# Optimization experiments

Hardware: AMD Instinct MI355X
Metric: run time of the kernel (lower is better)

Reference implementation:

```python
import jax, jax.numpy as jnp
import numpy as np

B, H, CI, O = 8, 16, 16, 16          # batch, child spatial, child caps, parent caps
K, S, ROUTINGS = 3, 1, 3             # kernel, stride, EM iterations
FINAL_LAMBDA = 0.01
EPS = 1e-9


def setup_inputs() -> dict:
    key = jax.random.key(0)
    k1, k2, k3, k4, k5 = jax.random.split(key, 5)
    inputs_pose = jax.random.normal(k1, (B, H, H, CI, 16), dtype=jnp.float32)
    inputs_activation = jax.random.uniform(k2, (B, H, H, CI, 1), dtype=jnp.float32)
    # transformation matrices: [1, k*k*child_caps, parent_caps, 4, 4]
    w = jax.random.normal(k3, (1, K * K * CI, O, 4, 4), dtype=jnp.float32)
    beta_a = jax.random.normal(k4, (O,), dtype=jnp.float32)
    beta_v = jax.random.normal(k5, (O,), dtype=jnp.float32)
    return {"inputs_pose": inputs_pose, "inputs_activation": inputs_activation,
            "w": w, "beta_a": beta_a, "beta_v": beta_v}


def _extract_patches(x, k, s):
    # kernel_tile: im2col-like gather. x: [B, H, W, ...] -> [B, p, p, k, k, ...]
    Hs = x.shape[1]
    p = (Hs - k) // s + 1
    idx = (jnp.arange(p) * s)[:, None] + jnp.arange(k)[None, :]      # [p, k]
    xh = x[:, idx]                   # [B, ph, kh, W, ...]
    patches = xh[:, :, :, idx]       # [B, ph, kh, pw, kw, ...]
    return jnp.swapaxes(patches, 2, 3), p


def _child_index_map(Hs, k, s, p):
    # flat child spatial index feeding each (parent pos, kernel slot)
    ph = np.arange(p)[:, None] * s + np.arange(k)[None, :]           # [p, k]
    ch = ph[:, None, :, None] * Hs + ph[None, :, None, :]            # [p, p, k, k]
    return ch.reshape(p * p, k * k)                                   # [P2, K2]


def reference(inputs_pose, inputs_activation, w, beta_a, beta_v):
    P = (H - K) // S + 1
    P2, K2 = P * P, K * K
    K2CI = K2 * CI

    # ---- kernel_tile ----
    pose_t, _ = _extract_patches(inputs_pose, K, S)       # [B,P,P,K,K,CI,16]
    act_t, _ = _extract_patches(inputs_activation, K, S)  # [B,P,P,K,K,CI,1]
    pose_unroll = pose_t.reshape(B * P2, K2CI, 4, 4)
    act_unroll = act_t.reshape(B * P2, K2CI)

    # ---- compute_votes: tiny 4x4 matmuls per (child slot, parent cap) ----
    votes = jnp.einsum('nkpq,koqr->nkopr', pose_unroll, w[0])  # [B*P2,K2CI,O,4,4]
    votes = votes.reshape(B, P2, K2CI, O, 16)
    act_i = act_unroll.reshape(B, P2, K2CI, 1, 1)

    # ---- spatial routing bookkeeping (static integers) ----
    child_idx = _child_index_map(H, K, S, P)                    # [P2, K2]
    kk_child = np.repeat(child_idx, CI, axis=1)                 # [P2, K2CI]
    counts = np.zeros(H * H, np.float32)
    np.add.at(counts, child_idx.reshape(-1), 1.0)               # parents per child pos
    cap_id = np.tile(np.arange(CI), K2)                         # [K2CI]
    seg = jnp.asarray((kk_child * CI + cap_id[None, :]).reshape(-1))  # [P2*K2CI]
    n_seg = H * H * CI

    # initial routing: uniform over all (parent pos, parent cap) each child feeds
    rr0 = 1.0 / (O * counts[kk_child])                          # [P2, K2CI]
    rr = jnp.asarray(rr0)[None, :, :, None, None]               # bcast [1,P2,K2CI,1,1]

    beta_a_b = beta_a.reshape(1, 1, 1, O, 1)
    beta_v_b = beta_v.reshape(1, 1, 1, O, 1)

    mean = act_j = None
    for it in range(ROUTINGS):
        inv_temp = FINAL_LAMBDA * (1.0 - 0.95 ** (it + 1))
        # ---- M-step: weighted Gaussian statistics ----
        rr_prime = rr * act_i                                   # [B,P2,K2CI,O,1]
        rr_sum = jnp.sum(rr_prime, axis=2, keepdims=True) + EPS # [B,P2,1,O,1]
        mean = jnp.sum(rr_prime * votes, axis=2, keepdims=True) / rr_sum
        var = jnp.sum(rr_prime * jnp.square(votes - mean), axis=2, keepdims=True) / rr_sum + EPS
        cost_h = (beta_v_b + 0.5 * jnp.log(var)) * rr_sum       # [B,P2,1,O,16]
        cost = jnp.sum(cost_h, axis=-1, keepdims=True)          # [B,P2,1,O,1]
        act_j = jax.nn.sigmoid(inv_temp * (beta_a_b - cost))    # [B,P2,1,O,1]
        # ---- E-step: softmax over all (parent pos, parent cap) per child capsule ----
        if it < ROUTINGS - 1:
            log_p = -0.5 * jnp.sum(jnp.square(votes - mean) / var
                                   + jnp.log(2.0 * np.pi * var), axis=-1)  # [B,P2,K2CI,O]
            zz = jnp.log(act_j[..., 0] + EPS) + log_p           # [B,P2,K2CI,O]
            z = jnp.transpose(zz, (1, 2, 0, 3)).reshape(P2 * K2CI, B, O)
            row_max = jnp.max(z, axis=-1)                       # [P2*K2CI, B]
            seg_max = jax.ops.segment_max(row_max, seg, num_segments=n_seg)
            g = seg_max[seg][..., None]
            ez = jnp.exp(z - g)
            denom = jax.ops.segment_sum(jnp.sum(ez, axis=-1), seg, num_segments=n_seg)[seg]
            rr_new = ez / (denom[..., None] + EPS)              # sums to 1 per child capsule
            rr = jnp.transpose(rr_new.reshape(P2, K2CI, B, O), (2, 0, 1, 3))[..., None]

    pose_out = mean[:, :, 0].reshape(B, P, P, O, 16)
    act_out = act_j[:, :, 0].reshape(B, P, P, O, 1)
    return pose_out, act_out
```

## Files before the change

### kernel.cpp

```cpp
#include <hip/hip_runtime.h>

namespace {
constexpr int B_ = 8, H_ = 16, CI_ = 16, O_ = 16, P_ = 14;
constexpr int P2_ = P_ * P_;
constexpr int K2CI_ = 144;
constexpr int NV_ = 2304;
constexpr float EPS_ = 1e-9f;
constexpr float LOG2PI_ = 1.8378770664093453f;

using f2 = __attribute__((ext_vector_type(2))) float;

__device__ __forceinline__ float cnt1(int h) {
  int lo = (h - (P_ - 1)) > 0 ? (h - (P_ - 1)) : 0;
  int hi = h < 2 ? h : 2;
  return (float)(hi - lo + 1);
}

__global__ __launch_bounds__(256) void transpose_w(const float* __restrict__ w,
                                                   float* __restrict__ wt) {
  const int i = blockIdx.x * 256 + threadIdx.x;
  const int ko = i >> 4, q = (i >> 2) & 3, r = i & 3;
  wt[(ko << 4) + (r << 2) + q] = w[i];
}

__global__ __launch_bounds__(256) void transpose_pose(const float* __restrict__ pose,
                                                      float* __restrict__ pose_t) {
  const int i = blockIdx.x * 256 + threadIdx.x;
  const int cell = i >> 4, idx = i & 15;
  const int p = idx >> 2, q = idx & 3;
  pose_t[(cell << 4) + (q << 2) + p] = pose[i];
}

__device__ __forceinline__ void vote_dot(const float* __restrict__ pb, const float4 w4,
                                         f2& v01, f2& v23) {
  const f2 A0 = *(const f2*)(pb + 0), B0 = *(const f2*)(pb + 2);
  const f2 A1 = *(const f2*)(pb + 4), B1 = *(const f2*)(pb + 6);
  const f2 A2 = *(const f2*)(pb + 8), B2 = *(const f2*)(pb + 10);
  const f2 A3 = *(const f2*)(pb + 12), B3 = *(const f2*)(pb + 14);
  v01 = A0 * w4.x;
  v23 = B0 * w4.x;
  v01 = __builtin_elementwise_fma(A1, (f2){w4.y, w4.y}, v01);
  v23 = __builtin_elementwise_fma(B1, (f2){w4.y, w4.y}, v23);
  v01 = __builtin_elementwise_fma(A2, (f2){w4.z, w4.z}, v01);
  v23 = __builtin_elementwise_fma(B2, (f2){w4.z, w4.z}, v23);
  v01 = __builtin_elementwise_fma(A3, (f2){w4.w, w4.w}, v01);
  v23 = __builtin_elementwise_fma(B3, (f2){w4.w, w4.w}, v23);
}

template <int MODE>
__global__ __launch_bounds__(512, 8) void caps_main(
    const float* __restrict__ pose_t, const float* __restrict__ act,
    const float* __restrict__ wt, const float* __restrict__ beta_a,
    const float* __restrict__ beta_v, const float* __restrict__ zin,
    const float* __restrict__ gmax, const float* __restrict__ gden,
    float* __restrict__ zout, float* __restrict__ out) {
  __shared__ float rr_s[(MODE == 0) ? K2CI_ : NV_];
  __shared__ f2 partv[4][512];
  __shared__ float partr[512];
  __shared__ f2 sfin[4][64];
  __shared__ float sfr[64];
  __shared__ float gm_s[(MODE == 0) ? 1 : K2CI_];
  __shared__ float ad_s[(MODE == 0) ? 1 : K2CI_];

  const int tid = threadIdx.x;
  const int wv = __builtin_amdgcn_readfirstlane(tid >> 6);
  const int l = tid & 63;
  const int o = l >> 2, r = l & 3;
  const int pid = blockIdx.x;
  const int b = pid / P2_;
  const int p2 = pid - b * P2_;
  const int pi = p2 / P_;
  const int pj = p2 - pi * P_;
  const float inv_temp = (MODE == 0) ? 0.0005f : (MODE == 1) ? 0.000975f : 0.00142625f;

  if (MODE == 0) {
    if (tid < K2CI_) {
      const int ci = tid & 15, kk = tid >> 4;
      const int ki = (kk >= 6) ? 2 : (kk >= 3) ? 1 : 0, kj = kk - 3 * ki;
      const int cidx = ((b * H_ + pi + ki) * H_ + pj + kj) * CI_ + ci;
      rr_s[tid] = act[cidx] / (16.0f * cnt1(pi + ki) * cnt1(pj + kj));
    }
  } else {
    if (tid < K2CI_) {
      const int ci = tid & 15, kk = tid >> 4;
      const int ki = (kk >= 6) ? 2 : (kk >= 3) ? 1 : 0, kj = kk - 3 * ki;
      const int cidx = ((b * H_ + pi + ki) * H_ + pj + kj) * CI_ + ci;
      gm_s[tid] = gmax[cidx];
      ad_s[tid] = act[cidx] / (gden[cidx] + EPS_);
    }
    __syncthreads();
    for (int i4 = tid; i4 < NV_ / 4; i4 += 512) {
      const float4 z4 = ((const float4*)(zin + (size_t)pid * NV_))[i4];
      const int k = i4 >> 2;
      const float gmk = gm_s[k], adk = ad_s[k];
      float4 r4;
      r4.x = __expf(z4.x - gmk) * adk;
      r4.y = __expf(z4.y - gmk) * adk;
      r4.z = __expf(z4.z - gmk) * adk;
      r4.w = __expf(z4.w - gmk) * adk;
      ((float4*)rr_s)[i4] = r4;
    }
  }
  __syncthreads();

  const float bvo = 16.0f * beta_v[o];
  const float bao = beta_a[o];

  const float* pose_b = pose_t + ((size_t)((b * H_ + pi) * H_ + pj) << 8);
  const float* wt_l = wt + (l << 2);
  const int ci0 = wv * 2;

  float prr = 0.f;
  f2 pm01 = {0.f, 0.f}, pm23 = {0.f, 0.f}, pv01 = {0.f, 0.f}, pv23 = {0.f, 0.f};
#pragma unroll
  for (int kk = 0; kk < 9; ++kk) {
    const int ki = kk / 3, kj = kk - 3 * (kk / 3);
    const float* pbase = pose_b + ((ki * H_ + kj) << 8);
    const float* wb = wt_l + ((size_t)kk << 12);
#pragma unroll
    for (int c = 0; c < 2; ++c) {
      const int ci = ci0 + c;
      const float4 w4 = *(const float4*)(wb + (ci << 8));
      f2 v01, v23;
      vote_dot(pbase + (ci << 4), w4, v01, v23);
      const float rrk =
          (MODE == 0) ? rr_s[kk * 16 + ci] : rr_s[((kk * 16 + ci) << 4) + o];
      prr += rrk;
      const f2 rr2 = {rrk, rrk};
      const f2 a01 = rr2 * v01, a23 = rr2 * v23;
      pm01 += a01;
      pm23 += a23;
      pv01 = __builtin_elementwise_fma(a01, v01, pv01);
      pv23 = __builtin_elementwise_fma(a23, v23, pv23);
    }
  }
  partv[0][tid] = pm01; partv[1][tid] = pm23;
  partv[2][tid] = pv01; partv[3][tid] = pv23;
  partr[tid] = prr;
  __syncthreads();
  if (tid < 320) {
    if (tid < 256) {
      const int st = tid >> 6, li = tid & 63;
      f2 acc = partv[st][li];
#pragma unroll
      for (int wvi = 1; wvi < 8; ++wvi) acc += partv[st][wvi * 64 + li];
      sfin[st][li] = acc;
    } else {
      const int li = tid & 63;
      float acc = partr[li];
#pragma unroll
      for (int wvi = 1; wvi < 8; ++wvi) acc += partr[wvi * 64 + li];
      sfr[li] = acc;
    }
  }
  __syncthreads();
  const f2 S01 = sfin[0][l], S23 = sfin[1][l];
  const f2 V01 = sfin[2][l], V23 = sfin[3][l];
  const float rsum = sfr[l] + EPS_;
  const float irs = 1.0f / rsum;
  const f2 irs2 = {irs, irs};
  const f2 m01 = S01 * irs2, m23 = S23 * irs2;
  const f2 zero2 = {0.f, 0.f}, eps2 = {EPS_, EPS_};
  const f2 va01 = __builtin_elementwise_max(V01 * irs2 - m01 * m01, zero2) + eps2;
  const f2 va23 = __builtin_elementwise_max(V23 * irs2 - m23 * m23, zero2) + eps2;
  float slv = __logf(va01.x) + __logf(va01.y) + __logf(va23.x) + __logf(va23.y);
  slv += __shfl_xor(slv, 1);
  slv += __shfl_xor(slv, 2);
  const float cost = (bvo + 0.5f * slv) * rsum;
  const float aj = 1.0f / (1.0f + __expf(-inv_temp * (bao - cost)));

  if (MODE == 2) {
    if (wv == 0) {
      float* ob = out + ((size_t)(pid * 16 + o) << 4) + r;
      ob[0] = m01.x; ob[4] = m01.y; ob[8] = m23.x; ob[12] = m23.y;
      if (r == 0) out[(size_t)B_ * P2_ * O_ * 16 + pid * 16 + o] = aj;
    }
    return;
  }

  const f2 iv01 = {1.0f / va01.x, 1.0f / va01.y};
  const f2 iv23 = {1.0f / va23.x, 1.0f / va23.y};
  const float Cz = __logf(aj + EPS_) - 0.5f * (slv + 16.0f * LOG2PI_);
  float* zo = zout + (size_t)pid * NV_ + o;
#pragma unroll
  for (int kk = 0; kk < 9; ++kk) {
    const int ki = kk / 3, kj = kk - 3 * (kk / 3);
    const float* pbase = pose_b + ((ki * H_ + kj) << 8);
    const float* wb = wt_l + ((size_t)kk << 12);
#pragma unroll
    for (int c = 0; c < 2; ++c) {
      const int ci = ci0 + c;
      const float4 w4 = *(const float4*)(wb + (ci << 8));
      f2 v01, v23;
      vote_dot(pbase + (ci << 4), w4, v01, v23);
      const f2 d01 = v01 - m01, d23 = v23 - m23;
      const f2 q2 = __builtin_elementwise_fma(d01 * d01, iv01, (d23 * d23) * iv23);
      float q = q2.x + q2.y;
      q += __shfl_xor(q, 1);
      q += __shfl_xor(q, 2);
      if (r == 0) zo[(kk * 16 + ci) << 4] = Cz - 0.5f * q;
    }
  }
}

__global__ __launch_bounds__(256) void seg_reduce(const float* __restrict__ z,
                                                  float* __restrict__ gmax,
                                                  float* __restrict__ gden) {
  const int tid = blockIdx.x * 256 + threadIdx.x;
  const int part = tid & 3, ci = (tid >> 2) & 15, w2 = (tid >> 6) & 15;
  const int h = (tid >> 10) & 15, b = tid >> 14;
  float4 v[9];
  float m = -3.0e38f;
#pragma unroll
  for (int s = 0; s < 9; ++s) {
    const int ki = (s >= 6) ? 2 : (s >= 3) ? 1 : 0, kj = s - 3 * ki;
    const int pi = h - ki, pj = w2 - kj;
    if ((unsigned)pi < (unsigned)P_ && (unsigned)pj < (unsigned)P_) {
      v[s] = *(const float4*)(z + (size_t)(b * P2_ + pi * P_ + pj) * NV_ + s * 256 +
                              ci * 16 + part * 4);
    } else {
      v[s] = make_float4(-3.0e38f, -3.0e38f, -3.0e38f, -3.0e38f);
    }
    m = fmaxf(m, fmaxf(fmaxf(v[s].x, v[s].y), fmaxf(v[s].z, v[s].w)));
  }
  m = fmaxf(m, __shfl_xor(m, 1));
  m = fmaxf(m, __shfl_xor(m, 2));
  float s_ = 0.f;
#pragma unroll
  for (int s = 0; s < 9; ++s) {
    s_ += __expf(v[s].x - m) + __expf(v[s].y - m) + __expf(v[s].z - m) + __expf(v[s].w - m);
  }
  s_ += __shfl_xor(s_, 1);
  s_ += __shfl_xor(s_, 2);
  if (part == 0) {
    gmax[tid >> 2] = m;
    gden[tid >> 2] = s_;
  }
}
}

extern "C" void kernel_launch(void* const* d_in, const int* in_sizes, int n_in,
                              void* d_out, int out_size, void* d_ws, size_t ws_size,
                              hipStream_t stream) {
  const float* pose = (const float*)d_in[0];
  const float* act = (const float*)d_in[1];
  const float* w = (const float*)d_in[2];
  const float* ba = (const float*)d_in[3];
  const float* bv = (const float*)d_in[4];
  float* out = (float*)d_out;

  float* z = (float*)d_ws;
  float* gm = z + (size_t)B_ * P2_ * NV_;
  float* gd = gm + B_ * H_ * H_ * CI_;
  float* wt = gd + B_ * H_ * H_ * CI_;
  float* pt = wt + 36864;

  const int NB = B_ * P2_;
  transpose_w<<<144, 256, 0, stream>>>(w, wt);
  transpose_pose<<<2048, 256, 0, stream>>>(pose, pt);
  caps_main<0><<<NB, 512, 0, stream>>>(pt, act, wt, ba, bv, z, gm, gd, z, out);
  seg_reduce<<<512, 256, 0, stream>>>(z, gm, gd);
  caps_main<1><<<NB, 512, 0, stream>>>(pt, act, wt, ba, bv, z, gm, gd, z, out);
  seg_reduce<<<512, 256, 0, stream>>>(z, gm, gd);
  caps_main<2><<<NB, 512, 0, stream>>>(pt, act, wt, ba, bv, z, gm, gd, z, out);
}
```

Before: 166.1 us.

## Merge transpose kernels and software-pipeline weight loads in vote loops

The two preprocessing transpose kernels are merged into one launch that branches on block index, removing one kernel launch. Both vote-computing loops in caps_main are flattened into a single 18-iteration loop. That loop prefetches the weight float4 two iterations ahead using double buffers and reads the pose as float4 instead of float2 pairs. The aim is to hide global load latency and cut launch overhead, at the cost of more live registers under the 512-thread, 8-wave launch bounds.

Measured after the change: 165.1 us. About the same (-0.6%).

```diff
diff --git a/kernel.cpp b/kernel.cpp
--- a/kernel.cpp
+++ b/kernel.cpp
@@ -16,35 +16,20 @@
   return (float)(hi - lo + 1);
 }
 
-__global__ __launch_bounds__(256) void transpose_w(const float* __restrict__ w,
-                                                   float* __restrict__ wt) {
-  const int i = blockIdx.x * 256 + threadIdx.x;
-  const int ko = i >> 4, q = (i >> 2) & 3, r = i & 3;
-  wt[(ko << 4) + (r << 2) + q] = w[i];
-}
-
-__global__ __launch_bounds__(256) void transpose_pose(const float* __restrict__ pose,
-                                                      float* __restrict__ pose_t) {
-  const int i = blockIdx.x * 256 + threadIdx.x;
-  const int cell = i >> 4, idx = i & 15;
-  const int p = idx >> 2, q = idx & 3;
-  pose_t[(cell << 4) + (q << 2) + p] = pose[i];
-}
-
-__device__ __forceinline__ void vote_dot(const float* __restrict__ pb, const float4 w4,
-                                         f2& v01, f2& v23) {
-  const f2 A0 = *(const f2*)(pb + 0), B0 = *(const f2*)(pb + 2);
-  const f2 A1 = *(const f2*)(pb + 4), B1 = *(const f2*)(pb + 6);
-  const f2 A2 = *(const f2*)(pb + 8), B2 = *(const f2*)(pb + 10);
-  const f2 A3 = *(const f2*)(pb + 12), B3 = *(const f2*)(pb + 14);
-  v01 = A0 * w4.x;
-  v23 = B0 * w4.x;
-  v01 = __builtin_elementwise_fma(A1, (f2){w4.y, w4.y}, v01);
-  v23 = __builtin_elementwise_fma(B1, (f2){w4.y, w4.y}, v23);
-  v01 = __builtin_elementwise_fma(A2, (f2){w4.z, w4.z}, v01);
-  v23 = __builtin_elementwise_fma(B2, (f2){w4.z, w4.z}, v23);
-  v01 = __builtin_elementwise_fma(A3, (f2){w4.w, w4.w}, v01);
-  v23 = __builtin_elementwise_fma(B3, (f2){w4.w, w4.w}, v23);
+__global__ __launch_bounds__(256) void transpose_all(const float* __restrict__ pose,
+                                                     float* __restrict__ pose_t,
+                                                     const float* __restrict__ w,
+                                                     float* __restrict__ wt) {
+  if (blockIdx.x < 2048) {
+    const int i = blockIdx.x * 256 + threadIdx.x;
+    const int cell = i >> 4, idx = i & 15;
+    const int p = idx >> 2, q = idx & 3;
+    pose_t[(cell << 4) + (q << 2) + p] = pose[i];
+  } else {
+    const int i = (blockIdx.x - 2048) * 256 + threadIdx.x;
+    const int ko = i >> 4, q = (i >> 2) & 3, r = i & 3;
+    wt[(ko << 4) + (r << 2) + q] = w[i];
+  }
 }
 
 template <int MODE>
@@ -110,21 +95,38 @@
   const float* wt_l = wt + (l << 2);
   const int ci0 = wv * 2;
 
+#define WT_OFF(idx) ((((idx) >> 1) << 12) + ((ci0 + ((idx)&1)) << 8))
+#define PB_OFF(idx) (((((idx) >> 1) / 3) << 12) + ((((idx) >> 1) % 3) << 8) + ((ci0 + ((idx)&1)) << 4))
+
   float prr = 0.f;
   f2 pm01 = {0.f, 0.f}, pm23 = {0.f, 0.f}, pv01 = {0.f, 0.f}, pv23 = {0.f, 0.f};
-#pragma unroll
-  for (int kk = 0; kk < 9; ++kk) {
-    const int ki = kk / 3, kj = kk - 3 * (kk / 3);
-    const float* pbase = pose_b + ((ki * H_ + kj) << 8);
-    const float* wb = wt_l + ((size_t)kk << 12);
-#pragma unroll
-    for (int c = 0; c < 2; ++c) {
-      const int ci = ci0 + c;
-      const float4 w4 = *(const float4*)(wb + (ci << 8));
-      f2 v01, v23;
-      vote_dot(pbase + (ci << 4), w4, v01, v23);
-      const float rrk =
-          (MODE == 0) ? rr_s[kk * 16 + ci] : rr_s[((kk * 16 + ci) << 4) + o];
+  {
+    float4 wbuf0 = *(const float4*)(wt_l + WT_OFF(0));
+    float4 wbuf1 = *(const float4*)(wt_l + WT_OFF(1));
+#pragma unroll
+    for (int idx = 0; idx < 18; ++idx) {
+      const float4 w4 = (idx & 1) ? wbuf1 : wbuf0;
+      if (idx < 16) {
+        if (idx & 1)
+          wbuf1 = *(const float4*)(wt_l + WT_OFF(idx + 2));
+        else
+          wbuf0 = *(const float4*)(wt_l + WT_OFF(idx + 2));
+      }
+      const float* pb = pose_b + PB_OFF(idx);
+      const float4 P0 = *(const float4*)(pb);
+      const float4 P1 = *(const float4*)(pb + 4);
+      const float4 P2 = *(const float4*)(pb + 8);
+      const float4 P3 = *(const float4*)(pb + 12);
+      f2 v01 = (f2){P0.x, P0.y} * w4.x;
+      f2 v23 = (f2){P0.z, P0.w} * w4.x;
+      v01 = __builtin_elementwise_fma((f2){P1.x, P1.y}, (f2){w4.y, w4.y}, v01);
+      v23 = __builtin_elementwise_fma((f2){P1.z, P1.w}, (f2){w4.y, w4.y}, v23);
+      v01 = __builtin_elementwise_fma((f2){P2.x, P2.y}, (f2){w4.z, w4.z}, v01);
+      v23 = __builtin_elementwise_fma((f2){P2.z, P2.w}, (f2){w4.z, w4.z}, v23);
+      v01 = __builtin_elementwise_fma((f2){P3.x, P3.y}, (f2){w4.w, w4.w}, v01);
+      v23 = __builtin_elementwise_fma((f2){P3.z, P3.w}, (f2){w4.w, w4.w}, v23);
+      const int k = ((idx >> 1) << 4) + ci0 + (idx & 1);
+      const float rrk = (MODE == 0) ? rr_s[k] : rr_s[(k << 4) + o];
       prr += rrk;
       const f2 rr2 = {rrk, rrk};
       const f2 a01 = rr2 * v01, a23 = rr2 * v23;
@@ -182,25 +184,42 @@
   const f2 iv23 = {1.0f / va23.x, 1.0f / va23.y};
   const float Cz = __logf(aj + EPS_) - 0.5f * (slv + 16.0f * LOG2PI_);
   float* zo = zout + (size_t)pid * NV_ + o;
-#pragma unroll
-  for (int kk = 0; kk < 9; ++kk) {
-    const int ki = kk / 3, kj = kk - 3 * (kk / 3);
-    const float* pbase = pose_b + ((ki * H_ + kj) << 8);
-    const float* wb = wt_l + ((size_t)kk << 12);
-#pragma unroll
-    for (int c = 0; c < 2; ++c) {
-      const int ci = ci0 + c;
-      const float4 w4 = *(const float4*)(wb + (ci << 8));
-      f2 v01, v23;
-      vote_dot(pbase + (ci << 4), w4, v01, v23);
+  {
+    float4 wbuf0 = *(const float4*)(wt_l + WT_OFF(0));
+    float4 wbuf1 = *(const float4*)(wt_l + WT_OFF(1));
+#pragma unroll
+    for (int idx = 0; idx < 18; ++idx) {
+      const float4 w4 = (idx & 1) ? wbuf1 : wbuf0;
+      if (idx < 16) {
+        if (idx & 1)
+          wbuf1 = *(const float4*)(wt_l + WT_OFF(idx + 2));
+        else
+          wbuf0 = *(const float4*)(wt_l + WT_OFF(idx + 2));
+      }
+      const float* pb = pose_b + PB_OFF(idx);
+      const float4 P0 = *(const float4*)(pb);
+      const float4 P1 = *(const float4*)(pb + 4);
+      const float4 P2 = *(const float4*)(pb + 8);
+      const float4 P3 = *(const float4*)(pb + 12);
+      f2 v01 = (f2){P0.x, P0.y} * w4.x;
+      f2 v23 = (f2){P0.z, P0.w} * w4.x;
+      v01 = __builtin_elementwise_fma((f2){P1.x, P1.y}, (f2){w4.y, w4.y}, v01);
+      v23 = __builtin_elementwise_fma((f2){P1.z, P1.w}, (f2){w4.y, w4.y}, v23);
+      v01 = __builtin_elementwise_fma((f2){P2.x, P2.y}, (f2){w4.z, w4.z}, v01);
+      v23 = __builtin_elementwise_fma((f2){P2.z, P2.w}, (f2){w4.z, w4.z}, v23);
+      v01 = __builtin_elementwise_fma((f2){P3.x, P3.y}, (f2){w4.w, w4.w}, v01);
+      v23 = __builtin_elementwise_fma((f2){P3.z, P3.w}, (f2){w4.w, w4.w}, v23);
       const f2 d01 = v01 - m01, d23 = v23 - m23;
       const f2 q2 = __builtin_elementwise_fma(d01 * d01, iv01, (d23 * d23) * iv23);
       float q = q2.x + q2.y;
       q += __shfl_xor(q, 1);
       q += __shfl_xor(q, 2);
-      if (r == 0) zo[(kk * 16 + ci) << 4] = Cz - 0.5f * q;
-    }
-  }
+      const int k = ((idx >> 1) << 4) + ci0 + (idx & 1);
+      if (r == 0) zo[k << 4] = Cz - 0.5f * q;
+    }
+  }
+#undef WT_OFF
+#undef PB_OFF
 }
 
 __global__ __launch_bounds__(256) void seg_reduce(const float* __restrict__ z,
@@ -256,8 +275,7 @@
   float* pt = wt + 36864;
 
   const int NB = B_ * P2_;
-  transpose_w<<<144, 256, 0, stream>>>(w, wt);
-  transpose_pose<<<2048, 256, 0, stream>>>(pose, pt);
+  transpose_all<<<2192, 256, 0, stream>>>(pose, pt, w, wt);
   caps_main<0><<<NB, 512, 0, stream>>>(pt, act, wt, ba, bv, z, gm, gd, z, out);
   seg_reduce<<<512, 256, 0, stream>>>(z, gm, gd);
   caps_main<1><<<NB, 512, 0, stream>>>(pt, act, wt, ba, bv, z, gm, gd, z, out);
```
